# Performance work log

Hardware: AMD Instinct MI355X
Metric: run time of the kernel (lower is better)

## Reference

```python
import jax, jax.numpy as jnp
import numpy as np

NEG_SLOPE = 0.2


def _gat_conv(x, edge_index, W, a_src, a_dst, b, heads, out_ch, concat):
    N = x.shape[0]
    # add self loops (PyG GATConv default)
    loops = jnp.arange(N, dtype=edge_index.dtype)
    src = jnp.concatenate([edge_index[0], loops])
    dst = jnp.concatenate([edge_index[1], loops])

    h = (x @ W).reshape(N, heads, out_ch)            # [N,H,C]
    alpha_s = jnp.einsum('nhc,hc->nh', h, a_src)     # [N,H]
    alpha_d = jnp.einsum('nhc,hc->nh', h, a_dst)     # [N,H]
    e = jax.nn.leaky_relu(alpha_s[src] + alpha_d[dst], NEG_SLOPE)  # [E,H]

    # softmax over incoming edges of each dst node (every node has a self loop)
    m = jax.ops.segment_max(e, dst, num_segments=N)  # [N,H]
    e = jnp.exp(e - m[dst])
    denom = jax.ops.segment_sum(e, dst, num_segments=N)  # [N,H]
    alpha = e / denom[dst]                           # [E,H]

    out = jax.ops.segment_sum(h[src] * alpha[..., None], dst, num_segments=N)  # [N,H,C]
    out = out.reshape(N, heads * out_ch) if concat else out.mean(axis=1)
    return out + b


def setup_inputs() -> dict:
    key = jax.random.key(0)
    ks = jax.random.split(key, 12)
    N, E = 100000, 3200000
    F_IN, HID, H1, H2, NCLS = 7, 8, 8, 1, 2
    x = jax.random.normal(ks[0], (N, F_IN), dtype=jnp.float32)
    edge_index = jax.random.randint(ks[1], (2, E), 0, N, dtype=jnp.int64)
    s1 = 1.0 / np.sqrt(F_IN)
    s2 = 1.0 / np.sqrt(HID * H1)
    return {
        'x': x,
        'edge_index': edge_index,
        'W1': jax.random.uniform(ks[2], (F_IN, H1 * HID), jnp.float32, -s1, s1),
        'a_src1': jax.random.uniform(ks[3], (H1, HID), jnp.float32, -s1, s1),
        'a_dst1': jax.random.uniform(ks[4], (H1, HID), jnp.float32, -s1, s1),
        'b1': jnp.zeros((H1 * HID,), jnp.float32),
        'W2': jax.random.uniform(ks[5], (H1 * HID, H2 * NCLS), jnp.float32, -s2, s2),
        'a_src2': jax.random.uniform(ks[6], (H2, NCLS), jnp.float32, -s2, s2),
        'a_dst2': jax.random.uniform(ks[7], (H2, NCLS), jnp.float32, -s2, s2),
        'b2': jnp.zeros((NCLS,), jnp.float32),
    }


def reference(x, edge_index, W1, a_src1, a_dst1, b1, W2, a_src2, a_dst2, b2):
    # eval mode: dropout is identity
    h = _gat_conv(x, edge_index, W1, a_src1, a_dst1, b1, heads=8, out_ch=8, concat=True)
    h = jax.nn.elu(h)
    out = _gat_conv(h, edge_index, W2, a_src2, a_dst2, b2, heads=1, out_ch=2, concat=False)
    return jax.nn.log_softmax(out, axis=1)
```

## Files before the change

### kernel.cpp

```cpp
#include <hip/hip_runtime.h>
#include <math.h>

#define NEG_SLOPE 0.2f
#define L2E 1.4426950408889634f
#define NPB_SHIFT 8
#define NBMAX 512
#define SC_EDGES 16384
#define SC_THREADS 1024
#define CAP 9216

__device__ __forceinline__ unsigned short f2bf(float f) {
    unsigned int u = __float_as_uint(f);
    u += 0x7FFFu + ((u >> 16) & 1u);
    return (unsigned short)(u >> 16);
}

__global__ void k_h1_scatter(const float* __restrict__ x, const float* __restrict__ W1,
                             const float* __restrict__ a_dst,
                             int N, char* __restrict__ rec,
                             float* __restrict__ ad1,
                             const int* __restrict__ srcA, const int* __restrict__ dstA,
                             int E, int sb, int* __restrict__ cursor_g,
                             unsigned int* __restrict__ payload) {
    __shared__ union {
        struct { int hist[NBMAX]; int gbase[NBMAX]; } sc;
        float ws[7 * 64];
    } smem;
    int t = threadIdx.x;

    if ((int)blockIdx.x < sb) {
        const int ITER = SC_EDGES / SC_THREADS;
        unsigned pay[ITER];
        int meta[ITER];
        int base = blockIdx.x * SC_EDGES;
        int cnt = E - base; if (cnt > SC_EDGES) cnt = SC_EDGES;
        for (int i = t; i < NBMAX; i += SC_THREADS) smem.sc.hist[i] = 0;
        __syncthreads();
#pragma unroll
        for (int k = 0; k < ITER; ++k) {
            int j = k * SC_THREADS + t;
            if (j < cnt) {
                int d = __builtin_nontemporal_load(dstA + base + j);
                int s = __builtin_nontemporal_load(srcA + base + j);
                int b = d >> NPB_SHIFT;
                pay[k] = ((unsigned int)(d & ((1 << NPB_SHIFT) - 1)) << 24) | (unsigned int)s;
                int r = atomicAdd(&smem.sc.hist[b], 1);
                meta[k] = (b << 15) | r;
            } else {
                meta[k] = -1;
            }
        }
        __syncthreads();
        for (int b = t; b < NBMAX; b += SC_THREADS) {
            int c = smem.sc.hist[b];
            smem.sc.gbase[b] = c ? atomicAdd(&cursor_g[b], c) : 0;
        }
        __syncthreads();
#pragma unroll
        for (int k = 0; k < ITER; ++k) {
            if (meta[k] >= 0) {
                int b = meta[k] >> 15;
                int r = meta[k] & 0x7FFF;
                int pos = smem.sc.gbase[b] + r;
                if ((unsigned)pos < CAP)
                    payload[(size_t)b * CAP + pos] = pay[k];
            }
        }
        return;
    }

    for (int i = t; i < 7 * 64; i += SC_THREADS) smem.ws[i] = W1[i];
    __syncthreads();
    int lane = t & 63;
    int base_n = (blockIdx.x - sb) * 64 + (t >> 6) * 4;
    float adv = a_dst[lane];
#pragma unroll
    for (int u = 0; u < 4; ++u) {
        int n = base_n + u;
        if (n >= N) break;
        float hv = 0.f;
#pragma unroll
        for (int k = 0; k < 7; ++k) hv += x[n * 7 + k] * smem.ws[k * 64 + lane];
        ((unsigned short*)(rec + ((size_t)n << 7)))[lane] = f2bf(hv);
        float pd = hv * adv;
#pragma unroll
        for (int off = 1; off < 8; off <<= 1) pd += __shfl_xor(pd, off);
        if ((lane & 7) == 0) ad1[n * 8 + (lane >> 3)] = pd * L2E;
    }
}

__global__ void k_buildcsr(const unsigned int* __restrict__ payload,
                           const int* __restrict__ cursor_g, int N,
                           int2* __restrict__ nrow, int* __restrict__ csr) {
    __shared__ int hist[256], exbase[256], scanb[256];
    const int ITER = (CAP + 1023) / 1024;
    unsigned p[ITER];
    int mt[ITER];
    int b = blockIdx.x;
    int t = threadIdx.x;
    int cntb = cursor_g[b]; if (cntb > CAP) cntb = CAP;
    int bs = b * CAP;
    int nodeBase = b << NPB_SHIFT;
    int nNodes = N - nodeBase; if (nNodes > 256) nNodes = 256;
    if (t < 256) hist[t] = 0;
    __syncthreads();
#pragma unroll
    for (int k = 0; k < ITER; ++k) {
        int i = k * 1024 + t;
        if (i < cntb) {
            p[k] = __builtin_nontemporal_load(payload + bs + i);
            int dl = p[k] >> 24;
            int r = atomicAdd(&hist[dl], 1);
            mt[k] = (dl << 14) | r;
        } else {
            mt[k] = -1;
        }
    }
    __syncthreads();
    if (t < 256) scanb[t] = hist[t];
    __syncthreads();
    for (int off = 1; off < 256; off <<= 1) {
        int u = 0;
        if (t < 256 && t >= off) u = scanb[t - off];
        __syncthreads();
        if (t < 256) scanb[t] += u;
        __syncthreads();
    }
    if (t < 256) {
        int own = hist[t];
        int ex = scanb[t] - own;
        exbase[t] = ex;
        if (t < nNodes) nrow[nodeBase + t] = make_int2(own, bs + ex);
    }
    __syncthreads();
#pragma unroll
    for (int k = 0; k < ITER; ++k) {
        if (mt[k] >= 0) {
            int dl = mt[k] >> 14;
            int r = mt[k] & 0x3FFF;
            csr[bs + exbase[dl] + r] = (int)(p[k] & 0xFFFFFFu);
        }
    }
}

__device__ __forceinline__ void oct_step(
    const char* __restrict__ rec, int s,
    unsigned foff, float4 awA, float4 awB,
    float adv, float wm, bool mask,
    float& den, float& a0, float& a1, float& a2, float& a3,
    float& a4, float& a5, float& a6, float& a7) {
    unsigned u = (unsigned)s;
    uint4 f = *(const uint4*)(rec + (size_t)((u << 7) + foff));
    float f0 = __uint_as_float(f.x << 16);
    float f1 = __uint_as_float(f.x & 0xFFFF0000u);
    float f2 = __uint_as_float(f.y << 16);
    float f3 = __uint_as_float(f.y & 0xFFFF0000u);
    float f4 = __uint_as_float(f.z << 16);
    float f5 = __uint_as_float(f.z & 0xFFFF0000u);
    float f6 = __uint_as_float(f.w << 16);
    float f7 = __uint_as_float(f.w & 0xFFFF0000u);
    float p = fmaf(f0, awA.x, adv);
    float q = f1 * awA.y;
    p = fmaf(f2, awA.z, p);
    q = fmaf(f3, awA.w, q);
    p = fmaf(f4, awB.x, p);
    q = fmaf(f5, awB.y, q);
    p = fmaf(f6, awB.z, p);
    q = fmaf(f7, awB.w, q);
    float t = p + q;
    float w = __builtin_amdgcn_exp2f(fmaxf(t, NEG_SLOPE * t));
    if (mask) w *= wm;
    den += w;
    a0 = fmaf(w, f0, a0);
    a1 = fmaf(w, f1, a1);
    a2 = fmaf(w, f2, a2);
    a3 = fmaf(w, f3, a3);
    a4 = fmaf(w, f4, a4);
    a5 = fmaf(w, f5, a5);
    a6 = fmaf(w, f6, a6);
    a7 = fmaf(w, f7, a7);
}

__global__ void k_agg1(const char* __restrict__ rec, const float* __restrict__ asW,
                       const float* __restrict__ ad1,
                       const int2* __restrict__ nrow,
                       const int* __restrict__ csr, const float* __restrict__ b1,
                       const float* __restrict__ W2, const float* __restrict__ as2w,
                       const float* __restrict__ ad2w, int N,
                       float4* __restrict__ pack) {
    int n = blockIdx.x * 4 + (threadIdx.x >> 6);
    int lane = threadIdx.x & 63;
    if (n >= N) return;
    n = __builtin_amdgcn_readfirstlane(n);
    int ql = lane & 7;
    int g  = lane >> 3;
    unsigned foff = (unsigned)(ql << 4);
    float4 awA = ((const float4*)asW)[2 * ql];
    float4 awB = ((const float4*)asW)[2 * ql + 1];
    awA.x *= L2E; awA.y *= L2E; awA.z *= L2E; awA.w *= L2E;
    awB.x *= L2E; awB.y *= L2E; awB.z *= L2E; awB.w *= L2E;
    float adv = ad1[n * 8 + ql];
    int2 dr = nrow[n];
    int d = __builtin_amdgcn_readfirstlane(dr.x);
    int start = __builtin_amdgcn_readfirstlane(dr.y);
    const int* csrg = csr + start + g;
    float a0 = 0.f, a1 = 0.f, a2 = 0.f, a3 = 0.f;
    float a4 = 0.f, a5 = 0.f, a6 = 0.f, a7 = 0.f;
    float den = 0.f;
    int c = 0;
    int nfull = d & ~31;
    for (; c < nfull; c += 32) {
#pragma unroll
        for (int k = 0; k < 4; ++k) {
            int s = csrg[c + 8 * k];
            oct_step(rec, s, foff, awA, awB, adv, 1.f, false,
                     den, a0, a1, a2, a3, a4, a5, a6, a7);
        }
    }
    for (; c < d; c += 8) {
        int pos = c + g;
        int cp = pos < d ? pos : d - 1;
        int s = csr[start + cp];
        float wm = pos < d ? 1.f : 0.f;
        oct_step(rec, s, foff, awA, awB, adv, wm, true,
                 den, a0, a1, a2, a3, a4, a5, a6, a7);
    }
    {
        float wm = (g == 0) ? 1.f : 0.f;
        oct_step(rec, n, foff, awA, awB, adv, wm, true,
                 den, a0, a1, a2, a3, a4, a5, a6, a7);
    }
    den += __shfl_xor(den, 8); den += __shfl_xor(den, 16); den += __shfl_xor(den, 32);
    a0 += __shfl_xor(a0, 8); a0 += __shfl_xor(a0, 16); a0 += __shfl_xor(a0, 32);
    a1 += __shfl_xor(a1, 8); a1 += __shfl_xor(a1, 16); a1 += __shfl_xor(a1, 32);
    a2 += __shfl_xor(a2, 8); a2 += __shfl_xor(a2, 16); a2 += __shfl_xor(a2, 32);
    a3 += __shfl_xor(a3, 8); a3 += __shfl_xor(a3, 16); a3 += __shfl_xor(a3, 32);
    a4 += __shfl_xor(a4, 8); a4 += __shfl_xor(a4, 16); a4 += __shfl_xor(a4, 32);
    a5 += __shfl_xor(a5, 8); a5 += __shfl_xor(a5, 16); a5 += __shfl_xor(a5, 32);
    a6 += __shfl_xor(a6, 8); a6 += __shfl_xor(a6, 16); a6 += __shfl_xor(a6, 32);
    a7 += __shfl_xor(a7, 8); a7 += __shfl_xor(a7, 16); a7 += __shfl_xor(a7, 32);
    float rden = 1.f / den;
    float4 bbA = ((const float4*)b1)[2 * ql];
    float4 bbB = ((const float4*)b1)[2 * ql + 1];
    float o0 = a0 * rden + bbA.x;
    float o1 = a1 * rden + bbA.y;
    float o2 = a2 * rden + bbA.z;
    float o3 = a3 * rden + bbA.w;
    float o4 = a4 * rden + bbB.x;
    float o5 = a5 * rden + bbB.y;
    float o6 = a6 * rden + bbB.z;
    float o7 = a7 * rden + bbB.w;
    float v0 = o0 > 0.f ? o0 : (__expf(o0) - 1.f);
    float v1 = o1 > 0.f ? o1 : (__expf(o1) - 1.f);
    float v2 = o2 > 0.f ? o2 : (__expf(o2) - 1.f);
    float v3 = o3 > 0.f ? o3 : (__expf(o3) - 1.f);
    float v4 = o4 > 0.f ? o4 : (__expf(o4) - 1.f);
    float v5 = o5 > 0.f ? o5 : (__expf(o5) - 1.f);
    float v6 = o6 > 0.f ? o6 : (__expf(o6) - 1.f);
    float v7 = o7 > 0.f ? o7 : (__expf(o7) - 1.f);
    const float4* W2v = (const float4*)W2;
    float4 w20 = W2v[4 * ql + 0];
    float4 w21 = W2v[4 * ql + 1];
    float4 w22 = W2v[4 * ql + 2];
    float4 w23 = W2v[4 * ql + 3];
    float p0 = v0 * w20.x + v1 * w20.z + v2 * w21.x + v3 * w21.z
             + v4 * w22.x + v5 * w22.z + v6 * w23.x + v7 * w23.z;
    float p1 = v0 * w20.y + v1 * w20.w + v2 * w21.y + v3 * w21.w
             + v4 * w22.y + v5 * w22.w + v6 * w23.y + v7 * w23.w;
#pragma unroll
    for (int off = 1; off < 8; off <<= 1) {
        p0 += __shfl_xor(p0, off);
        p1 += __shfl_xor(p1, off);
    }
    if (lane == 0) {
        float4 pk;
        pk.x = p0;
        pk.y = p1;
        pk.z = (p0 * as2w[0] + p1 * as2w[1]) * L2E;
        pk.w = (p0 * ad2w[0] + p1 * ad2w[1]) * L2E;
        pack[n] = pk;
    }
}

__global__ void k_agg2(const float4* __restrict__ pack, const int2* __restrict__ nrow,
                       const int* __restrict__ csr,
                       const float* __restrict__ b2, int N, float* __restrict__ out) {
    int n = blockIdx.x * 8 + (threadIdx.x >> 5);
    int hl = threadIdx.x & 31;
    if (n >= N) return;
    float4 self = pack[n];
    float adv = self.w;
    int2 dr = nrow[n];
    int d = dr.x;
    int start = dr.y;
    float den = 0.f, a0 = 0.f, a1 = 0.f;
    for (int i = hl; i < d; i += 32) {
        int src = __builtin_nontemporal_load(csr + start + i);
        float4 q = pack[src];
        float t = q.z + adv;
        float w = __builtin_amdgcn_exp2f(fmaxf(t, NEG_SLOPE * t));
        den += w;
        a0 += w * q.x;
        a1 += w * q.y;
    }
#pragma unroll
    for (int off = 1; off < 32; off <<= 1) {
        den += __shfl_xor(den, off);
        a0  += __shfl_xor(a0, off);
        a1  += __shfl_xor(a1, off);
    }
    if (hl == 0) {
        float t = self.z + adv;
        float w = __builtin_amdgcn_exp2f(fmaxf(t, NEG_SLOPE * t));
        den += w;
        a0 += w * self.x;
        a1 += w * self.y;
        float o0 = a0 / den + b2[0];
        float o1 = a1 / den + b2[1];
        float m = fmaxf(o0, o1);
        float lse = m + logf(__expf(o0 - m) + __expf(o1 - m));
        out[n * 2 + 0] = o0 - lse;
        out[n * 2 + 1] = o1 - lse;
    }
}

extern "C" void kernel_launch(void* const* d_in, const int* in_sizes, int n_in,
                              void* d_out, int out_size, void* d_ws, size_t ws_size,
                              hipStream_t stream) {
    const float* x     = (const float*)d_in[0];
    const int*   ei    = (const int*)d_in[1];
    const float* W1    = (const float*)d_in[2];
    const float* as1w  = (const float*)d_in[3];
    const float* ad1w  = (const float*)d_in[4];
    const float* b1    = (const float*)d_in[5];
    const float* W2    = (const float*)d_in[6];
    const float* as2w  = (const float*)d_in[7];
    const float* ad2w  = (const float*)d_in[8];
    const float* b2    = (const float*)d_in[9];
    float* out = (float*)d_out;

    const int N = in_sizes[0] / 7;
    const int E = in_sizes[1] / 2;
    const int* srcA = ei;
    const int* dstA = ei + E;
    const int NB = (N + ((1 << NPB_SHIFT) - 1)) >> NPB_SHIFT;

    size_t off = 0;
    auto alloc = [&](size_t bytes) -> void* {
        void* p = (char*)d_ws + off;
        off += (bytes + 255) & ~(size_t)255;
        return p;
    };
    unsigned int* payload = (unsigned int*)alloc((size_t)NB * CAP * 4);
    char*  rec  = (char*)alloc((size_t)N * 128);
    float* ad1  = (float*)alloc((size_t)N * 8 * 4);
    float4* pack = (float4*)alloc((size_t)N * 16);
    int2*  nrow = (int2*)alloc((size_t)N * 8);
    int*   csr  = (int*)alloc((size_t)NB * CAP * 4);
    int*   cursor_g = (int*)alloc(NBMAX * 4);

    const int nb2 = (N + 63) / 64;
    const int sb  = (E + SC_EDGES - 1) / SC_EDGES;
    const int nb  = (N + 3) / 4;

    hipMemsetAsync(cursor_g, 0, NBMAX * 4, stream);
    k_h1_scatter<<<sb + nb2, SC_THREADS, 0, stream>>>(x, W1, ad1w, N, rec, ad1,
                                                      srcA, dstA, E, sb, cursor_g, payload);
    k_buildcsr<<<NB, 1024, 0, stream>>>(payload, cursor_g, N, nrow, csr);
    k_agg1<<<nb, 256, 0, stream>>>(rec, as1w, ad1, nrow, csr, b1,
                                   W2, as2w, ad2w, N, pack);
    k_agg2<<<(N + 7) / 8, 256, 0, stream>>>(pack, nrow, csr, b2, N, out);
}
```

Baseline: 231.9 us.

## Process two destination nodes per wavefront in layer-1 aggregation

Layer-1 aggregation now gives each half-wavefront of 32 lanes its own destination node, so one wave handles two nodes instead of one. The edge loop is driven by the larger of the two degrees with per-lane masking, and reads 4 neighbours per step across 8 unrolled steps. The cross-lane reduction drops its 32-lane stage. This aims to use lanes better on low-degree nodes (average degree about 32) and to halve the number of waves, at the cost of divergence when the paired degrees differ and of extra masked work.

```diff
diff --git a/kernel.cpp b/kernel.cpp
--- a/kernel.cpp
+++ b/kernel.cpp
@@ -8,6 +8,8 @@
 #define SC_EDGES 16384
 #define SC_THREADS 1024
 #define CAP 9216
+
+typedef unsigned int u32x4 __attribute__((ext_vector_type(4)));
 
 __device__ __forceinline__ unsigned short f2bf(float f) {
     unsigned int u = __float_as_uint(f);
@@ -143,22 +145,18 @@
     }
 }
 
-__device__ __forceinline__ void oct_step(
-    const char* __restrict__ rec, int s,
-    unsigned foff, float4 awA, float4 awB,
-    float adv, float wm, bool mask,
+__device__ __forceinline__ void oct_core(
+    u32x4 f, float4 awA, float4 awB, float adv, float wm,
     float& den, float& a0, float& a1, float& a2, float& a3,
     float& a4, float& a5, float& a6, float& a7) {
-    unsigned u = (unsigned)s;
-    uint4 f = *(const uint4*)(rec + (size_t)((u << 7) + foff));
-    float f0 = __uint_as_float(f.x << 16);
-    float f1 = __uint_as_float(f.x & 0xFFFF0000u);
-    float f2 = __uint_as_float(f.y << 16);
-    float f3 = __uint_as_float(f.y & 0xFFFF0000u);
-    float f4 = __uint_as_float(f.z << 16);
-    float f5 = __uint_as_float(f.z & 0xFFFF0000u);
-    float f6 = __uint_as_float(f.w << 16);
-    float f7 = __uint_as_float(f.w & 0xFFFF0000u);
+    float f0 = __uint_as_float(f[0] << 16);
+    float f1 = __uint_as_float(f[0] & 0xFFFF0000u);
+    float f2 = __uint_as_float(f[1] << 16);
+    float f3 = __uint_as_float(f[1] & 0xFFFF0000u);
+    float f4 = __uint_as_float(f[2] << 16);
+    float f5 = __uint_as_float(f[2] & 0xFFFF0000u);
+    float f6 = __uint_as_float(f[3] << 16);
+    float f7 = __uint_as_float(f[3] & 0xFFFF0000u);
     float p = fmaf(f0, awA.x, adv);
     float q = f1 * awA.y;
     p = fmaf(f2, awA.z, p);
@@ -168,8 +166,7 @@
     p = fmaf(f6, awB.z, p);
     q = fmaf(f7, awB.w, q);
     float t = p + q;
-    float w = __builtin_amdgcn_exp2f(fmaxf(t, NEG_SLOPE * t));
-    if (mask) w *= wm;
+    float w = __builtin_amdgcn_exp2f(fmaxf(t, NEG_SLOPE * t)) * wm;
     den += w;
     a0 = fmaf(w, f0, a0);
     a1 = fmaf(w, f1, a1);
@@ -188,12 +185,13 @@
                        const float* __restrict__ W2, const float* __restrict__ as2w,
                        const float* __restrict__ ad2w, int N,
                        float4* __restrict__ pack) {
-    int n = blockIdx.x * 4 + (threadIdx.x >> 6);
     int lane = threadIdx.x & 63;
-    if (n >= N) return;
-    n = __builtin_amdgcn_readfirstlane(n);
+    int half = lane >> 5;
+    int n0 = blockIdx.x * 8 + (threadIdx.x >> 6) * 2 + half;
+    int n = n0 < N ? n0 : N - 1;
     int ql = lane & 7;
     int g  = lane >> 3;
+    int gsub = g & 3;
     unsigned foff = (unsigned)(ql << 4);
     float4 awA = ((const float4*)asW)[2 * ql];
     float4 awB = ((const float4*)asW)[2 * ql + 1];
@@ -201,44 +199,44 @@
     awB.x *= L2E; awB.y *= L2E; awB.z *= L2E; awB.w *= L2E;
     float adv = ad1[n * 8 + ql];
     int2 dr = nrow[n];
-    int d = __builtin_amdgcn_readfirstlane(dr.x);
-    int start = __builtin_amdgcn_readfirstlane(dr.y);
-    const int* csrg = csr + start + g;
+    int d = dr.x;
+    int start = dr.y;
+    const int* csrb = csr + start;
+    int dm1 = d - 1;
+    int dmx = max(d, __shfl_xor(d, 32));
+    int dmx_s = __builtin_amdgcn_readfirstlane(dmx);
     float a0 = 0.f, a1 = 0.f, a2 = 0.f, a3 = 0.f;
     float a4 = 0.f, a5 = 0.f, a6 = 0.f, a7 = 0.f;
     float den = 0.f;
-    int c = 0;
-    int nfull = d & ~31;
-    for (; c < nfull; c += 32) {
-#pragma unroll
-        for (int k = 0; k < 4; ++k) {
-            int s = csrg[c + 8 * k];
-            oct_step(rec, s, foff, awA, awB, adv, 1.f, false,
-                     den, a0, a1, a2, a3, a4, a5, a6, a7);
-        }
-    }
-    for (; c < d; c += 8) {
-        int pos = c + g;
-        int cp = pos < d ? pos : d - 1;
-        int s = csr[start + cp];
-        float wm = pos < d ? 1.f : 0.f;
-        oct_step(rec, s, foff, awA, awB, adv, wm, true,
+#define LDR(s) (*(const u32x4*)(rec + (size_t)((((unsigned)(s)) << 7) + foff)))
+    for (int c = 0; c < dmx_s; c += 32) {
+#pragma unroll
+        for (int k = 0; k < 8; ++k) {
+            if (c + 4 * k < dmx_s) {
+                int p = c + 4 * k + gsub;
+                int q = min(p, dm1);
+                int s = csrb[q];
+                float wm = (p < d) ? 1.f : 0.f;
+                oct_core(LDR(s), awA, awB, adv, wm,
+                         den, a0, a1, a2, a3, a4, a5, a6, a7);
+            }
+        }
+    }
+    {
+        float wm = (gsub == 0) ? 1.f : 0.f;
+        oct_core(LDR(n), awA, awB, adv, wm,
                  den, a0, a1, a2, a3, a4, a5, a6, a7);
     }
-    {
-        float wm = (g == 0) ? 1.f : 0.f;
-        oct_step(rec, n, foff, awA, awB, adv, wm, true,
-                 den, a0, a1, a2, a3, a4, a5, a6, a7);
-    }
-    den += __shfl_xor(den, 8); den += __shfl_xor(den, 16); den += __shfl_xor(den, 32);
-    a0 += __shfl_xor(a0, 8); a0 += __shfl_xor(a0, 16); a0 += __shfl_xor(a0, 32);
-    a1 += __shfl_xor(a1, 8); a1 += __shfl_xor(a1, 16); a1 += __shfl_xor(a1, 32);
-    a2 += __shfl_xor(a2, 8); a2 += __shfl_xor(a2, 16); a2 += __shfl_xor(a2, 32);
-    a3 += __shfl_xor(a3, 8); a3 += __shfl_xor(a3, 16); a3 += __shfl_xor(a3, 32);
-    a4 += __shfl_xor(a4, 8); a4 += __shfl_xor(a4, 16); a4 += __shfl_xor(a4, 32);
-    a5 += __shfl_xor(a5, 8); a5 += __shfl_xor(a5, 16); a5 += __shfl_xor(a5, 32);
-    a6 += __shfl_xor(a6, 8); a6 += __shfl_xor(a6, 16); a6 += __shfl_xor(a6, 32);
-    a7 += __shfl_xor(a7, 8); a7 += __shfl_xor(a7, 16); a7 += __shfl_xor(a7, 32);
+#undef LDR
+    den += __shfl_xor(den, 8); den += __shfl_xor(den, 16);
+    a0 += __shfl_xor(a0, 8); a0 += __shfl_xor(a0, 16);
+    a1 += __shfl_xor(a1, 8); a1 += __shfl_xor(a1, 16);
+    a2 += __shfl_xor(a2, 8); a2 += __shfl_xor(a2, 16);
+    a3 += __shfl_xor(a3, 8); a3 += __shfl_xor(a3, 16);
+    a4 += __shfl_xor(a4, 8); a4 += __shfl_xor(a4, 16);
+    a5 += __shfl_xor(a5, 8); a5 += __shfl_xor(a5, 16);
+    a6 += __shfl_xor(a6, 8); a6 += __shfl_xor(a6, 16);
+    a7 += __shfl_xor(a7, 8); a7 += __shfl_xor(a7, 16);
     float rden = 1.f / den;
     float4 bbA = ((const float4*)b1)[2 * ql];
     float4 bbB = ((const float4*)b1)[2 * ql + 1];
@@ -272,7 +270,7 @@
         p0 += __shfl_xor(p0, off);
         p1 += __shfl_xor(p1, off);
     }
-    if (lane == 0) {
+    if ((lane & 31) == 0 && n0 < N) {
         float4 pk;
         pk.x = p0;
         pk.y = p1;
@@ -361,7 +359,7 @@
 
     const int nb2 = (N + 63) / 64;
     const int sb  = (E + SC_EDGES - 1) / SC_EDGES;
-    const int nb  = (N + 3) / 4;
+    const int nb  = (N + 7) / 8;
 
     hipMemsetAsync(cursor_g, 0, NBMAX * 4, stream);
     k_h1_scatter<<<sb + nb2, SC_THREADS, 0, stream>>>(x, W1, ad1w, N, rec, ad1,
```

New measurement: 229.8 us. No clear change (-0.9%).
